# Kernel optimization log

Hardware: AMD Instinct MI355X
Metric: run time of the kernel (lower is better)

## Reference

```python
import jax, jax.numpy as jnp
import numpy as np

D = 256
RANK = 64
H = 8
DH = D // H
TOPK = 32  # top-k survivors per query row
NEG = -1e9


def lowrank(x, u, v):
    # x:[...,d] @ u:[d,rank] @ v:[rank,d]
    return (x @ u) @ v


def setup_inputs() -> dict:
    key = jax.random.key(0)
    ks = jax.random.split(key, 13)
    s_u = 1.0 / np.sqrt(D)
    s_v = 1.0 / np.sqrt(RANK)

    def pu(k):
        return jax.random.normal(k, (D, RANK), jnp.float32) * s_u

    def pv(k):
        return jax.random.normal(k, (RANK, D), jnp.float32) * s_v

    return {
        "x": jax.random.normal(ks[0], (2, 2048, D), jnp.float32),
        "ne_u": pu(ks[1]), "ne_v": pv(ks[2]),
        "wq_u": pu(ks[3]), "wq_v": pv(ks[4]),
        "wk_u": pu(ks[5]), "wk_v": pv(ks[6]),
        "wv_u": pu(ks[7]), "wv_v": pv(ks[8]),
        "wo_u": pu(ks[9]), "wo_v": pv(ks[10]),
        "es_u": pu(ks[11]), "es_v": pv(ks[12]),
    }


def reference(x, ne_u, ne_v, wq_u, wq_v, wk_u, wk_v, wv_u, wv_v, wo_u, wo_v, es_u, es_v):
    B, N, _ = x.shape
    # node embedding (low-rank projection)
    h = lowrank(x, ne_u, ne_v)  # [B,N,d]

    # low-rank multi-head Q/K/V
    def heads(t):  # [B,N,d] -> [B,H,N,dh]
        return t.reshape(B, N, H, DH).transpose(0, 2, 1, 3)

    q = heads(lowrank(h, wq_u, wq_v))
    k = heads(lowrank(h, wk_u, wk_v))
    v = heads(lowrank(h, wv_u, wv_v))

    scores = jnp.einsum("bhnd,bhmd->bhnm", q, k) / jnp.sqrt(jnp.float32(DH))
    # top-k sparsification per query row
    kth = jax.lax.top_k(scores, TOPK)[0][..., -1:]  # [B,H,N,1]
    masked = jnp.where(scores >= kth, scores, NEG)
    attn = jax.nn.softmax(masked, axis=-1)  # [B,H,N,N]

    out = jnp.einsum("bhnm,bhmd->bhnd", attn, v)  # [B,H,N,dh]
    out = out.transpose(0, 2, 1, 3).reshape(B, N, D)
    h2 = lowrank(out, wo_u, wo_v)  # output projection

    # edge scores -> adjacency with sigmoid + zero diagonal epilogue
    el = lowrank(h2, es_u, es_v)  # [B,N,d]
    adjacency = jax.nn.sigmoid(jnp.einsum("bnd,bmd->bnm", el, el))
    adjacency = adjacency * (1.0 - jnp.eye(N, dtype=adjacency.dtype))
    return adjacency, attn
```

## Files before the change

kernel.cpp:

```cpp
#include <hip/hip_runtime.h>
#include <hip/hip_bf16.h>
#include <cstdint>
#include <cstddef>

#define ATTN_OFF (2u*2048u*2048u)
#define SLOTS 48
#define DELTA 1e-3f
#define MAXB 16
#define CCAP 96

typedef __attribute__((ext_vector_type(8))) short bf16x8;
typedef __attribute__((ext_vector_type(4))) float f32x4;

__device__ __forceinline__ unsigned short bf16_hi(float f) {
  __hip_bfloat16 h = __float2bfloat16(f);
  return *(unsigned short*)&h;
}
__device__ __forceinline__ float bf16_val(unsigned short u) {
  __hip_bfloat16 h = *(__hip_bfloat16*)&u;
  return __bfloat162float(h);
}

__global__ __launch_bounds__(256) void fused_qkv_kernel(
    const float* __restrict__ x, const float* __restrict__ ne_u,
    const float* __restrict__ ne_v, const float* __restrict__ wq_u,
    const float* __restrict__ wq_v, const float* __restrict__ wk_u,
    const float* __restrict__ wk_v, const float* __restrict__ wv_u,
    const float* __restrict__ wv_v, double* __restrict__ qd,
    double* __restrict__ kd, unsigned short* __restrict__ qh,
    unsigned short* __restrict__ ql, unsigned short* __restrict__ kh,
    unsigned short* __restrict__ kl, float* __restrict__ v) {
  __shared__ double xm[4][64];
  __shared__ double hrow[4][256];
  __shared__ double mid2[4][64];

  int tid = threadIdx.x;
  int rr = tid >> 6;
  int j  = tid & 63;
  int row = blockIdx.x * 4 + rr;
  int b = row >> 11, m = row & 2047;
  const double INV = 0.17677669529663688110021109052621;

  const float* xr = x + (size_t)row * 256;
  {
    double a0 = 0, a1 = 0, a2 = 0, a3 = 0;
#pragma unroll 8
    for (int k4 = 0; k4 < 64; ++k4) {
      int kk = k4 * 4;
      a0 = fma((double)xr[kk + 0], (double)ne_u[(kk + 0) * 64 + j], a0);
      a1 = fma((double)xr[kk + 1], (double)ne_u[(kk + 1) * 64 + j], a1);
      a2 = fma((double)xr[kk + 2], (double)ne_u[(kk + 2) * 64 + j], a2);
      a3 = fma((double)xr[kk + 3], (double)ne_u[(kk + 3) * 64 + j], a3);
    }
    xm[rr][j] = (a0 + a1) + (a2 + a3);
  }
  __syncthreads();

#pragma unroll
  for (int cc = 0; cc < 4; ++cc) {
    int col = j + 64 * cc;
    double o0 = 0, o1 = 0, o2 = 0, o3 = 0;
#pragma unroll 4
    for (int r4 = 0; r4 < 16; ++r4) {
      int r = r4 * 4;
      o0 = fma(xm[rr][r + 0], (double)ne_v[(r + 0) * 256 + col], o0);
      o1 = fma(xm[rr][r + 1], (double)ne_v[(r + 1) * 256 + col], o1);
      o2 = fma(xm[rr][r + 2], (double)ne_v[(r + 2) * 256 + col], o2);
      o3 = fma(xm[rr][r + 3], (double)ne_v[(r + 3) * 256 + col], o3);
    }
    hrow[rr][col] = (o0 + o1) + (o2 + o3);
  }
  __syncthreads();

  for (int p = 0; p < 3; ++p) {
    const float* pu = (p == 0) ? wq_u : (p == 1) ? wk_u : wv_u;
    const float* pw = (p == 0) ? wq_v : (p == 1) ? wk_v : wv_v;

    double a0 = 0, a1 = 0, a2 = 0, a3 = 0;
#pragma unroll 8
    for (int k4 = 0; k4 < 64; ++k4) {
      int kk = k4 * 4;
      a0 = fma(hrow[rr][kk + 0], (double)pu[(kk + 0) * 64 + j], a0);
      a1 = fma(hrow[rr][kk + 1], (double)pu[(kk + 1) * 64 + j], a1);
      a2 = fma(hrow[rr][kk + 2], (double)pu[(kk + 2) * 64 + j], a2);
      a3 = fma(hrow[rr][kk + 3], (double)pu[(kk + 3) * 64 + j], a3);
    }
    mid2[rr][j] = (a0 + a1) + (a2 + a3);
    __syncthreads();

#pragma unroll
    for (int cc = 0; cc < 4; ++cc) {
      int col = j + 64 * cc;
      double o0 = 0, o1 = 0, o2 = 0, o3 = 0;
#pragma unroll 4
      for (int r4 = 0; r4 < 16; ++r4) {
        int r = r4 * 4;
        o0 = fma(mid2[rr][r + 0], (double)pw[(r + 0) * 256 + col], o0);
        o1 = fma(mid2[rr][r + 1], (double)pw[(r + 1) * 256 + col], o1);
        o2 = fma(mid2[rr][r + 2], (double)pw[(r + 2) * 256 + col], o2);
        o3 = fma(mid2[rr][r + 3], (double)pw[(r + 3) * 256 + col], o3);
      }
      double o = (o0 + o1) + (o2 + o3);
      if (p == 2) {
        v[(size_t)row * 256 + col] = (float)o;
      } else {
        int hh = col >> 5, d = col & 31;
        size_t haddr = (((size_t)(b * 8 + hh)) * 2048 + m) * 32 + d;
        if (p == 0) {
          qd[(size_t)row * 256 + col] = o;
          float f = (float)(o * INV);
          unsigned short hi = bf16_hi(f);
          float lof = f - bf16_val(hi);
          qh[haddr] = hi;
          ql[haddr] = bf16_hi(lof);
        } else {
          kd[(size_t)row * 256 + col] = o;
          float f = (float)o;
          unsigned short hi = bf16_hi(f);
          float lof = f - bf16_val(hi);
          kh[haddr] = hi;
          kl[haddr] = bf16_hi(lof);
        }
      }
    }
    __syncthreads();
  }
}

__global__ __launch_bounds__(512, 4) void attn_kernel(
    const unsigned short* __restrict__ qh, const unsigned short* __restrict__ ql,
    const unsigned short* __restrict__ kh, const unsigned short* __restrict__ kl,
    const double* __restrict__ qd, const double* __restrict__ kd,
    float* __restrict__ attn, float* __restrict__ pval,
    unsigned short* __restrict__ pidx) {
  __shared__ unsigned hist[16][64];
  __shared__ float cand[16][CCAP];
  __shared__ float sval[16][SLOTS];
  __shared__ unsigned short scol[16][SLOTS];
  __shared__ float rowmax_s[16][8];
  __shared__ unsigned c1_s[16][8];
  __shared__ unsigned c2_s[16][8];
  __shared__ float mx_s[16];
  __shared__ float kth_s[16];
  __shared__ float zinv_s[16];
  __shared__ float scale_s[16];
  __shared__ float thr_s[16];
  __shared__ int   kB_s[16];
  __shared__ unsigned kneed_s[16];
  __shared__ unsigned ccnt[16];
  __shared__ unsigned scnt[16];
  __shared__ unsigned chi_s[16];
  __shared__ unsigned bcnt[16];
  __shared__ unsigned short bidx[16][MAXB];
  __shared__ float bval[16][MAXB];
  __shared__ unsigned short bkeep[16][MAXB];
  __shared__ double bs64[16][MAXB];

  int tid = threadIdx.x;
  int bx  = blockIdx.x;
  int slab = bx >> 7;
  int rowtile = bx & 127;
  int b = slab >> 3, hh = slab & 7;
  int w = tid >> 6;
  int l = tid & 63;
  int g = l >> 4;
  int li = l & 15;
  const double INV64 = 0.17677669529663688110021109052621;

  size_t qoff = (((size_t)slab * 2048 + rowtile * 16 + li) * 32) + g * 8;
  bf16x8 a_hi = *(const bf16x8*)(qh + qoff);
  bf16x8 a_lo = *(const bf16x8*)(ql + qoff);

  float s[16][4];
  size_t kbase = ((size_t)slab * 2048 + w * 256 + li) * 32 + g * 8;
#pragma unroll
  for (int tt = 0; tt < 16; ++tt) {
    bf16x8 b_hi = *(const bf16x8*)(kh + kbase + (size_t)tt * 512);
    bf16x8 b_lo = *(const bf16x8*)(kl + kbase + (size_t)tt * 512);
    f32x4 acc = {0.f, 0.f, 0.f, 0.f};
    acc = __builtin_amdgcn_mfma_f32_16x16x32_bf16(a_hi, b_hi, acc, 0, 0, 0);
    acc = __builtin_amdgcn_mfma_f32_16x16x32_bf16(a_hi, b_lo, acc, 0, 0, 0);
    acc = __builtin_amdgcn_mfma_f32_16x16x32_bf16(a_lo, b_hi, acc, 0, 0, 0);
#pragma unroll
    for (int reg = 0; reg < 4; ++reg) s[tt][reg] = acc[reg];
  }

  for (int i = tid; i < 16 * 64; i += 512) ((unsigned*)hist)[i] = 0u;
  if (tid < 16) {
    ccnt[tid] = 0u; scnt[tid] = 0u; chi_s[tid] = 0u; bcnt[tid] = 0u;
    kth_s[tid] = -1e30f; kB_s[tid] = -1;
  }
  size_t prow0 = ((size_t)slab * 2048 + rowtile * 16);
  {
    float lmx[4];
#pragma unroll
    for (int reg = 0; reg < 4; ++reg) {
      float m = s[0][reg];
#pragma unroll
      for (int tt = 1; tt < 16; ++tt) m = fmaxf(m, s[tt][reg]);
      lmx[reg] = m;
    }
#pragma unroll
    for (int off = 1; off < 16; off <<= 1) {
#pragma unroll
      for (int reg = 0; reg < 4; ++reg)
        lmx[reg] = fmaxf(lmx[reg], __shfl_xor(lmx[reg], (unsigned)off, 16));
    }
    if (li == 0) {
#pragma unroll
      for (int reg = 0; reg < 4; ++reg) rowmax_s[4 * g + reg][w] = lmx[reg];
    }
  }
  __syncthreads();

  if (tid < 16) {
    float m = rowmax_s[tid][0];
#pragma unroll
    for (int i = 1; i < 8; ++i) m = fmaxf(m, rowmax_s[tid][i]);
    mx_s[tid] = m;
  }
  __syncthreads();

  {
    unsigned cc1[4], cc2[4];
#pragma unroll
    for (int reg = 0; reg < 4; ++reg) {
      float mx = mx_s[4 * g + reg];
      float t1 = mx - 1.0f, t2 = mx - 2.0f;
      unsigned a = 0, c = 0;
#pragma unroll
      for (int tt = 0; tt < 16; ++tt) {
        float v = s[tt][reg];
        a += (v >= t1) ? 1u : 0u;
        c += (v >= t2) ? 1u : 0u;
      }
      cc1[reg] = a; cc2[reg] = c;
    }
#pragma unroll
    for (int off = 1; off < 16; off <<= 1) {
#pragma unroll
      for (int reg = 0; reg < 4; ++reg) {
        cc1[reg] += (unsigned)__shfl_xor((int)cc1[reg], off, 16);
        cc2[reg] += (unsigned)__shfl_xor((int)cc2[reg], off, 16);
      }
    }
    if (li == 0) {
#pragma unroll
      for (int reg = 0; reg < 4; ++reg) {
        c1_s[4 * g + reg][w] = cc1[reg];
        c2_s[4 * g + reg][w] = cc2[reg];
      }
    }
  }
  __syncthreads();

  if (tid < 16) {
    unsigned t1 = 0, t2 = 0;
#pragma unroll
    for (int i = 0; i < 8; ++i) { t1 += c1_s[tid][i]; t2 += c2_s[tid][i]; }
    float scale, thr;
    if (t1 >= 32u)      { scale = 64.0f; thr = mx_s[tid] - 1.0f; }
    else if (t2 >= 32u) { scale = 32.0f; thr = mx_s[tid] - 2.0f; }
    else                { scale = 4.0f;  thr = -1e30f; }
    scale_s[tid] = scale; thr_s[tid] = thr;
  }
  __syncthreads();

#pragma unroll
  for (int reg = 0; reg < 4; ++reg) {
    int rloc = 4 * g + reg;
    float mx = mx_s[rloc], thr = thr_s[rloc], sc = scale_s[rloc];
#pragma unroll
    for (int tt = 0; tt < 16; ++tt) {
      float v = s[tt][reg];
      if (v >= thr) {
        int bb = (int)((mx - v) * sc);
        bb = bb > 63 ? 63 : bb;
        atomicAdd(&hist[rloc][bb], 1u);
      }
    }
  }
  __syncthreads();

  if (w < 4) {
    int rloc = w * 4 + g;
    unsigned cnt4 = 0;
#pragma unroll
    for (int i = 0; i < 4; ++i) cnt4 += hist[rloc][li * 4 + i];
    unsigned pre = cnt4;
#pragma unroll
    for (int off = 1; off < 16; off <<= 1) {
      unsigned t = __shfl_up(pre, (unsigned)off, 16);
      if (li >= off) pre += t;
    }
    unsigned excl = pre - cnt4;
    bool flag = (excl < 32u) && (pre >= 32u);
    unsigned long long bal = __ballot(flag);
    unsigned seg = (unsigned)((bal >> (g * 16)) & 0xFFFFull);
    if (flag) {
      int src = __ffs(seg) - 1;
      if (li == src) {
        unsigned cum = excl;
        int B = 63; unsigned cb = 0;
#pragma unroll
        for (int i = 0; i < 4; ++i) {
          unsigned hv = hist[rloc][li * 4 + i];
          if (cum < 32u && cum + hv >= 32u) { B = li * 4 + i; cb = cum; }
          cum += hv;
        }
        kB_s[rloc] = B;
        kneed_s[rloc] = 32u - cb;
      }
    }
  }
  __syncthreads();

#pragma unroll
  for (int reg = 0; reg < 4; ++reg) {
    int rloc = 4 * g + reg;
    float mx = mx_s[rloc], thr = thr_s[rloc], sc = scale_s[rloc];
    int kB = kB_s[rloc];
#pragma unroll
    for (int tt = 0; tt < 16; ++tt) {
      float v = s[tt][reg];
      if (v >= thr) {
        int bb = (int)((mx - v) * sc);
        bb = bb > 63 ? 63 : bb;
        if (bb == kB) {
          unsigned slot = atomicAdd(&ccnt[rloc], 1u);
          if (slot < (unsigned)CCAP) cand[rloc][slot] = v;
        }
      }
    }
  }
  __syncthreads();

  if (w < 4) {
    int rloc = w * 4 + g;
    unsigned n0 = ccnt[rloc];
    n0 = n0 > (unsigned)CCAP ? (unsigned)CCAP : n0;
    unsigned need = kneed_s[rloc];
    if (need > n0) need = n0;
    for (unsigned ci = (unsigned)li; ci < n0; ci += 16u) {
      float x = cand[rloc][ci];
      unsigned r = 0;
      for (unsigned jj = 0; jj < n0; ++jj) {
        float y = cand[rloc][jj];
        r += (y > x || (y == x && jj < ci)) ? 1u : 0u;
      }
      if (r == need - 1u) kth_s[rloc] = x;
    }
  }
  __syncthreads();

#pragma unroll
  for (int reg = 0; reg < 4; ++reg) {
    int rloc = 4 * g + reg;
    float kth = kth_s[rloc];
    unsigned cnt = 0;
#pragma unroll
    for (int tt = 0; tt < 16; ++tt) {
      float v = s[tt][reg];
      if (v > kth + DELTA) {
        ++cnt;
        unsigned slot = atomicAdd(&scnt[rloc], 1u);
        if (slot < (unsigned)SLOTS) {
          sval[rloc][slot] = v;
          scol[rloc][slot] = (unsigned short)(w * 256 + tt * 16 + li);
        }
      } else if (!(v < kth - DELTA)) {
        unsigned slot = atomicAdd(&bcnt[rloc], 1u);
        if (slot < (unsigned)MAXB) {
          bidx[rloc][slot] = (unsigned short)(w * 256 + tt * 16 + li);
          bval[rloc][slot] = v;
        }
      }
    }
#pragma unroll
    for (int off = 1; off < 16; off <<= 1)
      cnt += (unsigned)__shfl_xor((int)cnt, off, 16);
    if (li == 0) atomicAdd(&chi_s[rloc], cnt);
  }
  __syncthreads();

  if (w < 4) {
    int rloc = w * 4 + g;
    unsigned bn = bcnt[rloc];
    bn = bn > (unsigned)MAXB ? (unsigned)MAXB : bn;
    const double* qrow =
        qd + ((size_t)(b * 2048 + rowtile * 16 + rloc)) * 256 + hh * 32;
    for (unsigned ci = (unsigned)li; ci < bn; ci += 16u) {
      int m = bidx[rloc][ci];
      const double* krow = kd + ((size_t)(b * 2048 + m)) * 256 + hh * 32;
      double acc = 0.0;
#pragma unroll 8
      for (int d = 0; d < 32; ++d) acc = fma(qrow[d], krow[d], acc);
      bs64[rloc][ci] = acc * INV64;
    }
    unsigned need2 = 32u - chi_s[rloc];
    for (unsigned ci = (unsigned)li; ci < bn; ci += 16u) {
      double x = bs64[rloc][ci];
      unsigned r = 0;
      for (unsigned jj = 0; jj < bn; ++jj)
        r += (bs64[rloc][jj] > x) ? 1u : 0u;
      if (r < need2) {
        unsigned slot = atomicAdd(&scnt[rloc], 1u);
        if (slot < (unsigned)SLOTS) {
          sval[rloc][slot] = bval[rloc][ci];
          scol[rloc][slot] = bidx[rloc][ci];
        }
      }
    }
  }
  __syncthreads();

  float* base = attn + prow0 * 2048;
  if (w < 4) {
    int rloc = w * 4 + g;
    unsigned n = scnt[rloc];
    n = n > (unsigned)SLOTS ? (unsigned)SLOTS : n;
    float mx = mx_s[rloc];
    float z = 0.0f;
    for (unsigned i = (unsigned)li; i < n; i += 16u)
      z += __expf(sval[rloc][i] - mx);
#pragma unroll
    for (int off = 1; off < 16; off <<= 1) z += __shfl_xor(z, (unsigned)off, 16);
    if (li == 0) zinv_s[rloc] = 1.0f / z;
  } else {
    int t2 = tid - 256;
    f32x4 z4 = {0.f, 0.f, 0.f, 0.f};
#pragma unroll
    for (int it = 0; it < 32; ++it)
      __builtin_nontemporal_store(z4, ((f32x4*)base) + t2 + 256 * it);
  }
  __syncthreads();

  for (int e = tid; e < 16 * SLOTS; e += 512) {
    int rr = e / SLOTS, ii = e % SLOTS;
    unsigned n = scnt[rr];
    n = n > (unsigned)SLOTS ? (unsigned)SLOTS : n;
    float p = 0.0f;
    unsigned short c = 0;
    if ((unsigned)ii < n) {
      c = scol[rr][ii];
      p = __expf(sval[rr][ii] - mx_s[rr]) * zinv_s[rr];
      base[(size_t)rr * 2048 + c] = p;
    }
    pval[prow0 * SLOTS + e] = p;
    pidx[prow0 * SLOTS + e] = c;
  }
}

__global__ __launch_bounds__(256) void pv_wo_es_kernel(
    const float* __restrict__ pval, const unsigned short* __restrict__ pidx,
    const float* __restrict__ v,
    const float* __restrict__ wo_u, const float* __restrict__ wo_v,
    const float* __restrict__ es_u, const float* __restrict__ es_v,
    unsigned short* __restrict__ elh, unsigned short* __restrict__ ell) {
  __shared__ float svals[8][8][SLOTS];
  __shared__ unsigned short sidx[8][8][SLOTS];
  __shared__ float outr[8][256];
  __shared__ float mid[8][64];
  __shared__ float h2r[8][256];

  int tid = threadIdx.x;
  int bb = blockIdx.x >> 8;
  int rg = blockIdx.x & 255;
  int n0 = rg * 8;

  for (int e = tid; e < 8 * 8 * SLOTS; e += 256) {
    int rr = e / (8 * SLOTS);
    int rem = e % (8 * SLOTS);
    int hh = rem / SLOTS, ii = rem % SLOTS;
    size_t srow = ((size_t)(bb * 8 + hh) * 2048 + n0 + rr) * SLOTS + ii;
    svals[rr][hh][ii] = pval[srow];
    sidx[rr][hh][ii] = pidx[srow];
  }
  __syncthreads();

  {
    int d = tid, hh = d >> 5;
    const float* vb = v + (size_t)bb * 2048 * 256 + d;
    for (int r = 0; r < 8; ++r) {
      float acc = 0.f;
#pragma unroll 4
      for (int i = 0; i < SLOTS; ++i) {
        float p = svals[r][hh][i];
        int m = sidx[r][hh][i];
        acc = fmaf(p, vb[(size_t)m * 256], acc);
      }
      outr[r][d] = acc;
    }
  }
  __syncthreads();

  {
    int j = tid & 63, rb = tid >> 6;
    for (int r = rb; r < 8; r += 4) {
      float a0 = 0, a1 = 0, a2 = 0, a3 = 0;
#pragma unroll 8
      for (int k4 = 0; k4 < 64; ++k4) {
        int k = k4 * 4;
        a0 = fmaf(outr[r][k + 0], wo_u[(k + 0) * 64 + j], a0);
        a1 = fmaf(outr[r][k + 1], wo_u[(k + 1) * 64 + j], a1);
        a2 = fmaf(outr[r][k + 2], wo_u[(k + 2) * 64 + j], a2);
        a3 = fmaf(outr[r][k + 3], wo_u[(k + 3) * 64 + j], a3);
      }
      mid[r][j] = (a0 + a1) + (a2 + a3);
    }
  }
  __syncthreads();

  {
    int c = tid;
    for (int r = 0; r < 8; ++r) {
      float a0 = 0, a1 = 0, a2 = 0, a3 = 0;
#pragma unroll 4
      for (int k4 = 0; k4 < 16; ++k4) {
        int k = k4 * 4;
        a0 = fmaf(mid[r][k + 0], wo_v[(k + 0) * 256 + c], a0);
        a1 = fmaf(mid[r][k + 1], wo_v[(k + 1) * 256 + c], a1);
        a2 = fmaf(mid[r][k + 2], wo_v[(k + 2) * 256 + c], a2);
        a3 = fmaf(mid[r][k + 3], wo_v[(k + 3) * 256 + c], a3);
      }
      h2r[r][c] = (a0 + a1) + (a2 + a3);
    }
  }
  __syncthreads();

  {
    int j = tid & 63, rb = tid >> 6;
    for (int r = rb; r < 8; r += 4) {
      float a0 = 0, a1 = 0, a2 = 0, a3 = 0;
#pragma unroll 8
      for (int k4 = 0; k4 < 64; ++k4) {
        int k = k4 * 4;
        a0 = fmaf(h2r[r][k + 0], es_u[(k + 0) * 64 + j], a0);
        a1 = fmaf(h2r[r][k + 1], es_u[(k + 1) * 64 + j], a1);
        a2 = fmaf(h2r[r][k + 2], es_u[(k + 2) * 64 + j], a2);
        a3 = fmaf(h2r[r][k + 3], es_u[(k + 3) * 64 + j], a3);
      }
      mid[r][j] = (a0 + a1) + (a2 + a3);
    }
  }
  __syncthreads();

  {
    int c = tid;
    for (int r = 0; r < 8; ++r) {
      float a0 = 0, a1 = 0, a2 = 0, a3 = 0;
#pragma unroll 4
      for (int k4 = 0; k4 < 16; ++k4) {
        int k = k4 * 4;
        a0 = fmaf(mid[r][k + 0], es_v[(k + 0) * 256 + c], a0);
        a1 = fmaf(mid[r][k + 1], es_v[(k + 1) * 256 + c], a1);
        a2 = fmaf(mid[r][k + 2], es_v[(k + 2) * 256 + c], a2);
        a3 = fmaf(mid[r][k + 3], es_v[(k + 3) * 256 + c], a3);
      }
      float o = (a0 + a1) + (a2 + a3);
      size_t addr = ((size_t)(bb * 2048 + n0 + r)) * 256 + c;
      unsigned short hi = bf16_hi(o);
      elh[addr] = hi;
      ell[addr] = bf16_hi(o - bf16_val(hi));
    }
  }
}

__global__ __launch_bounds__(256) void adj_mfma_kernel(
    const unsigned short* __restrict__ elh, const unsigned short* __restrict__ ell,
    float* __restrict__ adj) {
  int tid = threadIdx.x;
  int l = tid & 63, w = tid >> 6;
  int li = l & 15, g = l >> 4;
  int b = blockIdx.z, rt = blockIdx.y, ct = blockIdx.x;

  int arow = rt * 64 + w * 16 + li;
  size_t abase = ((size_t)(b * 2048 + arow)) * 256 + g * 8;
  size_t bbase = ((size_t)(b * 2048 + ct * 64 + li)) * 256 + g * 8;

  f32x4 acc0 = {0.f, 0.f, 0.f, 0.f};
  f32x4 acc1 = {0.f, 0.f, 0.f, 0.f};
  f32x4 acc2 = {0.f, 0.f, 0.f, 0.f};
  f32x4 acc3 = {0.f, 0.f, 0.f, 0.f};

#pragma unroll
  for (int kc = 0; kc < 8; ++kc) {
    bf16x8 a_hi = *(const bf16x8*)(elh + abase + kc * 32);
    bf16x8 a_lo = *(const bf16x8*)(ell + abase + kc * 32);
#pragma unroll
    for (int t = 0; t < 4; ++t) {
      bf16x8 b_hi = *(const bf16x8*)(elh + bbase + (size_t)t * 16 * 256 + kc * 32);
      bf16x8 b_lo = *(const bf16x8*)(ell + bbase + (size_t)t * 16 * 256 + kc * 32);
      f32x4* pa = (t == 0) ? &acc0 : (t == 1) ? &acc1 : (t == 2) ? &acc2 : &acc3;
      *pa = __builtin_amdgcn_mfma_f32_16x16x32_bf16(a_hi, b_hi, *pa, 0, 0, 0);
      *pa = __builtin_amdgcn_mfma_f32_16x16x32_bf16(a_hi, b_lo, *pa, 0, 0, 0);
      *pa = __builtin_amdgcn_mfma_f32_16x16x32_bf16(a_lo, b_hi, *pa, 0, 0, 0);
    }
  }

  int orow0 = rt * 64 + w * 16 + g * 4;
#pragma unroll
  for (int t = 0; t < 4; ++t) {
    f32x4 a = (t == 0) ? acc0 : (t == 1) ? acc1 : (t == 2) ? acc2 : acc3;
    int cg = ct * 64 + t * 16 + li;
#pragma unroll
    for (int i = 0; i < 4; ++i) {
      int rg = orow0 + i;
      float sg = 1.0f / (1.0f + __expf(-a[i]));
      if (rg == cg) sg = 0.0f;
      adj[((size_t)b * 2048 + rg) * 2048 + cg] = sg;
    }
  }
}

extern "C" void kernel_launch(void* const* d_in, const int* in_sizes, int n_in,
                              void* d_out, int out_size, void* d_ws,
                              size_t ws_size, hipStream_t stream) {
  const float* x    = (const float*)d_in[0];
  const float* ne_u = (const float*)d_in[1];
  const float* ne_v = (const float*)d_in[2];
  const float* wq_u = (const float*)d_in[3];
  const float* wq_v = (const float*)d_in[4];
  const float* wk_u = (const float*)d_in[5];
  const float* wk_v = (const float*)d_in[6];
  const float* wv_u = (const float*)d_in[7];
  const float* wv_v = (const float*)d_in[8];
  const float* wo_u = (const float*)d_in[9];
  const float* wo_v = (const float*)d_in[10];
  const float* es_u = (const float*)d_in[11];
  const float* es_v = (const float*)d_in[12];

  float* adj  = (float*)d_out;
  float* attn = adj + (size_t)ATTN_OFF;

  char* ws = (char*)d_ws;
  double* qd = (double*)(ws);
  double* kd = (double*)(ws + ((size_t)8  << 20));
  unsigned short* qh = (unsigned short*)(ws + ((size_t)16 << 20));
  unsigned short* ql = (unsigned short*)(ws + ((size_t)18 << 20));
  unsigned short* kh = (unsigned short*)(ws + ((size_t)20 << 20));
  unsigned short* kl = (unsigned short*)(ws + ((size_t)22 << 20));
  float* v    = (float*)(ws + ((size_t)24 << 20));
  float* pval = (float*)(ws + ((size_t)28 << 20));
  unsigned short* pidx = (unsigned short*)(ws + ((size_t)35 << 20));
  unsigned short* elh = (unsigned short*)(ws + ((size_t)8  << 20));
  unsigned short* ell = (unsigned short*)(ws + ((size_t)10 << 20));

  fused_qkv_kernel<<<1024, 256, 0, stream>>>(
      x, ne_u, ne_v, wq_u, wq_v, wk_u, wk_v, wv_u, wv_v,
      qd, kd, qh, ql, kh, kl, v);

  attn_kernel<<<2048, 512, 0, stream>>>(qh, ql, kh, kl, qd, kd, attn, pval, pidx);
  pv_wo_es_kernel<<<512, 256, 0, stream>>>(pval, pidx, v, wo_u, wo_v,
                                           es_u, es_v, elh, ell);

  adj_mfma_kernel<<<dim3(32, 32, 2), 256, 0, stream>>>(elh, ell, adj);
}
```

Before: 395.7 us.

## Spread per-row top-k selection across all waves and halve rows per PV block

In the attention kernel, the threshold-count reduction now uses shared-memory atomics, so one barrier and a serial tid<16 pass go away. The histogram scan, candidate ranking, fp64 rescoring and softmax now run on all 8 waves with 32 lanes per row instead of 4 waves with 16 lanes. Exp values are cached in shared memory and reused for the normalised write, and the zero-fill of the output is spread across all threads. The PV/output-projection kernel processes 4 rows per block instead of 8, doubling the grid for more parallelism, at the cost of reloading the weights more often.

```diff
diff --git a/kernel.cpp b/kernel.cpp
--- a/kernel.cpp
+++ b/kernel.cpp
@@ -7,7 +7,8 @@
 #define SLOTS 48
 #define DELTA 1e-3f
 #define MAXB 16
-#define CCAP 96
+#define CCAP 64
+#define PVR 4
 
 typedef __attribute__((ext_vector_type(8))) short bf16x8;
 typedef __attribute__((ext_vector_type(4))) float f32x4;
@@ -138,22 +139,18 @@
   __shared__ float sval[16][SLOTS];
   __shared__ unsigned short scol[16][SLOTS];
   __shared__ float rowmax_s[16][8];
-  __shared__ unsigned c1_s[16][8];
-  __shared__ unsigned c2_s[16][8];
   __shared__ float mx_s[16];
   __shared__ float kth_s[16];
   __shared__ float zinv_s[16];
-  __shared__ float scale_s[16];
-  __shared__ float thr_s[16];
   __shared__ int   kB_s[16];
   __shared__ unsigned kneed_s[16];
+  __shared__ unsigned c1t[16], c2t[16];
   __shared__ unsigned ccnt[16];
   __shared__ unsigned scnt[16];
   __shared__ unsigned chi_s[16];
   __shared__ unsigned bcnt[16];
   __shared__ unsigned short bidx[16][MAXB];
   __shared__ float bval[16][MAXB];
-  __shared__ unsigned short bkeep[16][MAXB];
   __shared__ double bs64[16][MAXB];
 
   int tid = threadIdx.x;
@@ -165,6 +162,9 @@
   int l = tid & 63;
   int g = l >> 4;
   int li = l & 15;
+  int h32 = l >> 5;
+  int c32 = l & 31;
+  int rw = w * 2 + h32;
   const double INV64 = 0.17677669529663688110021109052621;
 
   size_t qoff = (((size_t)slab * 2048 + rowtile * 16 + li) * 32) + g * 8;
@@ -188,6 +188,7 @@
   for (int i = tid; i < 16 * 64; i += 512) ((unsigned*)hist)[i] = 0u;
   if (tid < 16) {
     ccnt[tid] = 0u; scnt[tid] = 0u; chi_s[tid] = 0u; bcnt[tid] = 0u;
+    c1t[tid] = 0u; c2t[tid] = 0u;
     kth_s[tid] = -1e30f; kB_s[tid] = -1;
   }
   size_t prow0 = ((size_t)slab * 2048 + rowtile * 16);
@@ -222,10 +223,10 @@
   __syncthreads();
 
   {
-    unsigned cc1[4], cc2[4];
 #pragma unroll
     for (int reg = 0; reg < 4; ++reg) {
-      float mx = mx_s[4 * g + reg];
+      int rloc = 4 * g + reg;
+      float mx = mx_s[rloc];
       float t1 = mx - 1.0f, t2 = mx - 2.0f;
       unsigned a = 0, c = 0;
 #pragma unroll
@@ -234,42 +235,28 @@
         a += (v >= t1) ? 1u : 0u;
         c += (v >= t2) ? 1u : 0u;
       }
-      cc1[reg] = a; cc2[reg] = c;
-    }
-#pragma unroll
-    for (int off = 1; off < 16; off <<= 1) {
-#pragma unroll
-      for (int reg = 0; reg < 4; ++reg) {
-        cc1[reg] += (unsigned)__shfl_xor((int)cc1[reg], off, 16);
-        cc2[reg] += (unsigned)__shfl_xor((int)cc2[reg], off, 16);
-      }
-    }
-    if (li == 0) {
-#pragma unroll
-      for (int reg = 0; reg < 4; ++reg) {
-        c1_s[4 * g + reg][w] = cc1[reg];
-        c2_s[4 * g + reg][w] = cc2[reg];
-      }
-    }
-  }
-  __syncthreads();
-
-  if (tid < 16) {
-    unsigned t1 = 0, t2 = 0;
-#pragma unroll
-    for (int i = 0; i < 8; ++i) { t1 += c1_s[tid][i]; t2 += c2_s[tid][i]; }
-    float scale, thr;
-    if (t1 >= 32u)      { scale = 64.0f; thr = mx_s[tid] - 1.0f; }
-    else if (t2 >= 32u) { scale = 32.0f; thr = mx_s[tid] - 2.0f; }
-    else                { scale = 4.0f;  thr = -1e30f; }
-    scale_s[tid] = scale; thr_s[tid] = thr;
+#pragma unroll
+      for (int off = 1; off < 16; off <<= 1) {
+        a += (unsigned)__shfl_xor((int)a, off, 16);
+        c += (unsigned)__shfl_xor((int)c, off, 16);
+      }
+      if (li == 0) {
+        if (a) atomicAdd(&c1t[rloc], a);
+        if (c) atomicAdd(&c2t[rloc], c);
+      }
+    }
   }
   __syncthreads();
 
 #pragma unroll
   for (int reg = 0; reg < 4; ++reg) {
     int rloc = 4 * g + reg;
-    float mx = mx_s[rloc], thr = thr_s[rloc], sc = scale_s[rloc];
+    float mx = mx_s[rloc];
+    unsigned t1 = c1t[rloc], t2 = c2t[rloc];
+    float sc, thr;
+    if (t1 >= 32u)      { sc = 64.0f; thr = mx - 1.0f; }
+    else if (t2 >= 32u) { sc = 32.0f; thr = mx - 2.0f; }
+    else                { sc = 4.0f;  thr = -1e30f; }
 #pragma unroll
     for (int tt = 0; tt < 16; ++tt) {
       float v = s[tt][reg];
@@ -282,34 +269,31 @@
   }
   __syncthreads();
 
-  if (w < 4) {
-    int rloc = w * 4 + g;
-    unsigned cnt4 = 0;
-#pragma unroll
-    for (int i = 0; i < 4; ++i) cnt4 += hist[rloc][li * 4 + i];
-    unsigned pre = cnt4;
-#pragma unroll
-    for (int off = 1; off < 16; off <<= 1) {
-      unsigned t = __shfl_up(pre, (unsigned)off, 16);
-      if (li >= off) pre += t;
-    }
-    unsigned excl = pre - cnt4;
+  {
+    unsigned cnt2 = hist[rw][c32 * 2] + hist[rw][c32 * 2 + 1];
+    unsigned pre = cnt2;
+#pragma unroll
+    for (int off = 1; off < 32; off <<= 1) {
+      unsigned t = __shfl_up(pre, (unsigned)off, 32);
+      if (c32 >= off) pre += t;
+    }
+    unsigned excl = pre - cnt2;
     bool flag = (excl < 32u) && (pre >= 32u);
     unsigned long long bal = __ballot(flag);
-    unsigned seg = (unsigned)((bal >> (g * 16)) & 0xFFFFull);
+    unsigned seg = (unsigned)((bal >> (h32 * 32)) & 0xFFFFFFFFull);
     if (flag) {
       int src = __ffs(seg) - 1;
-      if (li == src) {
+      if (c32 == src) {
         unsigned cum = excl;
         int B = 63; unsigned cb = 0;
 #pragma unroll
-        for (int i = 0; i < 4; ++i) {
-          unsigned hv = hist[rloc][li * 4 + i];
-          if (cum < 32u && cum + hv >= 32u) { B = li * 4 + i; cb = cum; }
+        for (int i = 0; i < 2; ++i) {
+          unsigned hv = hist[rw][c32 * 2 + i];
+          if (cum < 32u && cum + hv >= 32u) { B = c32 * 2 + i; cb = cum; }
           cum += hv;
         }
-        kB_s[rloc] = B;
-        kneed_s[rloc] = 32u - cb;
+        kB_s[rw] = B;
+        kneed_s[rw] = 32u - cb;
       }
     }
   }
@@ -318,7 +302,12 @@
 #pragma unroll
   for (int reg = 0; reg < 4; ++reg) {
     int rloc = 4 * g + reg;
-    float mx = mx_s[rloc], thr = thr_s[rloc], sc = scale_s[rloc];
+    float mx = mx_s[rloc];
+    unsigned t1 = c1t[rloc], t2 = c2t[rloc];
+    float sc, thr;
+    if (t1 >= 32u)      { sc = 64.0f; thr = mx - 1.0f; }
+    else if (t2 >= 32u) { sc = 32.0f; thr = mx - 2.0f; }
+    else                { sc = 4.0f;  thr = -1e30f; }
     int kB = kB_s[rloc];
 #pragma unroll
     for (int tt = 0; tt < 16; ++tt) {
@@ -335,20 +324,19 @@
   }
   __syncthreads();
 
-  if (w < 4) {
-    int rloc = w * 4 + g;
-    unsigned n0 = ccnt[rloc];
+  {
+    unsigned n0 = ccnt[rw];
     n0 = n0 > (unsigned)CCAP ? (unsigned)CCAP : n0;
-    unsigned need = kneed_s[rloc];
+    unsigned need = kneed_s[rw];
     if (need > n0) need = n0;
-    for (unsigned ci = (unsigned)li; ci < n0; ci += 16u) {
-      float x = cand[rloc][ci];
+    for (unsigned ci = (unsigned)c32; ci < n0; ci += 32u) {
+      float x = cand[rw][ci];
       unsigned r = 0;
       for (unsigned jj = 0; jj < n0; ++jj) {
-        float y = cand[rloc][jj];
+        float y = cand[rw][jj];
         r += (y > x || (y == x && jj < ci)) ? 1u : 0u;
       }
-      if (r == need - 1u) kth_s[rloc] = x;
+      if (r == need - 1u) kth_s[rw] = x;
     }
   }
   __syncthreads();
@@ -379,35 +367,34 @@
 #pragma unroll
     for (int off = 1; off < 16; off <<= 1)
       cnt += (unsigned)__shfl_xor((int)cnt, off, 16);
-    if (li == 0) atomicAdd(&chi_s[rloc], cnt);
-  }
-  __syncthreads();
-
-  if (w < 4) {
-    int rloc = w * 4 + g;
-    unsigned bn = bcnt[rloc];
+    if (li == 0 && cnt) atomicAdd(&chi_s[rloc], cnt);
+  }
+  __syncthreads();
+
+  {
+    unsigned bn = bcnt[rw];
     bn = bn > (unsigned)MAXB ? (unsigned)MAXB : bn;
     const double* qrow =
-        qd + ((size_t)(b * 2048 + rowtile * 16 + rloc)) * 256 + hh * 32;
-    for (unsigned ci = (unsigned)li; ci < bn; ci += 16u) {
-      int m = bidx[rloc][ci];
+        qd + ((size_t)(b * 2048 + rowtile * 16 + rw)) * 256 + hh * 32;
+    for (unsigned ci = (unsigned)c32; ci < bn; ci += 32u) {
+      int m = bidx[rw][ci];
       const double* krow = kd + ((size_t)(b * 2048 + m)) * 256 + hh * 32;
       double acc = 0.0;
 #pragma unroll 8
       for (int d = 0; d < 32; ++d) acc = fma(qrow[d], krow[d], acc);
-      bs64[rloc][ci] = acc * INV64;
-    }
-    unsigned need2 = 32u - chi_s[rloc];
-    for (unsigned ci = (unsigned)li; ci < bn; ci += 16u) {
-      double x = bs64[rloc][ci];
+      bs64[rw][ci] = acc * INV64;
+    }
+    unsigned need2 = 32u - chi_s[rw];
+    for (unsigned ci = (unsigned)c32; ci < bn; ci += 32u) {
+      double x = bs64[rw][ci];
       unsigned r = 0;
       for (unsigned jj = 0; jj < bn; ++jj)
-        r += (bs64[rloc][jj] > x) ? 1u : 0u;
+        r += (bs64[rw][jj] > x) ? 1u : 0u;
       if (r < need2) {
-        unsigned slot = atomicAdd(&scnt[rloc], 1u);
+        unsigned slot = atomicAdd(&scnt[rw], 1u);
         if (slot < (unsigned)SLOTS) {
-          sval[rloc][slot] = bval[rloc][ci];
-          scol[rloc][slot] = bidx[rloc][ci];
+          sval[rw][slot] = bval[rw][ci];
+          scol[rw][slot] = bidx[rw][ci];
         }
       }
     }
@@ -415,23 +402,25 @@
   __syncthreads();
 
   float* base = attn + prow0 * 2048;
-  if (w < 4) {
-    int rloc = w * 4 + g;
-    unsigned n = scnt[rloc];
+  {
+    unsigned n = scnt[rw];
     n = n > (unsigned)SLOTS ? (unsigned)SLOTS : n;
-    float mx = mx_s[rloc];
+    float mx = mx_s[rw];
     float z = 0.0f;
-    for (unsigned i = (unsigned)li; i < n; i += 16u)
-      z += __expf(sval[rloc][i] - mx);
-#pragma unroll
-    for (int off = 1; off < 16; off <<= 1) z += __shfl_xor(z, (unsigned)off, 16);
-    if (li == 0) zinv_s[rloc] = 1.0f / z;
-  } else {
-    int t2 = tid - 256;
+    for (unsigned i = (unsigned)c32; i < n; i += 32u) {
+      float e = __expf(sval[rw][i] - mx);
+      sval[rw][i] = e;
+      z += e;
+    }
+#pragma unroll
+    for (int off = 1; off < 32; off <<= 1) z += __shfl_xor(z, (unsigned)off, 32);
+    if (c32 == 0) zinv_s[rw] = 1.0f / z;
+  }
+  {
     f32x4 z4 = {0.f, 0.f, 0.f, 0.f};
 #pragma unroll
-    for (int it = 0; it < 32; ++it)
-      __builtin_nontemporal_store(z4, ((f32x4*)base) + t2 + 256 * it);
+    for (int it = 0; it < 16; ++it)
+      __builtin_nontemporal_store(z4, ((f32x4*)base) + tid + 512 * it);
   }
   __syncthreads();
 
@@ -443,7 +432,7 @@
     unsigned short c = 0;
     if ((unsigned)ii < n) {
       c = scol[rr][ii];
-      p = __expf(sval[rr][ii] - mx_s[rr]) * zinv_s[rr];
+      p = sval[rr][ii] * zinv_s[rr];
       base[(size_t)rr * 2048 + c] = p;
     }
     pval[prow0 * SLOTS + e] = p;
@@ -457,18 +446,18 @@
     const float* __restrict__ wo_u, const float* __restrict__ wo_v,
     const float* __restrict__ es_u, const float* __restrict__ es_v,
     unsigned short* __restrict__ elh, unsigned short* __restrict__ ell) {
-  __shared__ float svals[8][8][SLOTS];
-  __shared__ unsigned short sidx[8][8][SLOTS];
-  __shared__ float outr[8][256];
-  __shared__ float mid[8][64];
-  __shared__ float h2r[8][256];
+  __shared__ float svals[PVR][8][SLOTS];
+  __shared__ unsigned short sidx[PVR][8][SLOTS];
+  __shared__ float outr[PVR][256];
+  __shared__ float mid[PVR][64];
+  __shared__ float h2r[PVR][256];
 
   int tid = threadIdx.x;
-  int bb = blockIdx.x >> 8;
-  int rg = blockIdx.x & 255;
-  int n0 = rg * 8;
-
-  for (int e = tid; e < 8 * 8 * SLOTS; e += 256) {
+  int bb = blockIdx.x >> 9;
+  int rg = blockIdx.x & 511;
+  int n0 = rg * PVR;
+
+  for (int e = tid; e < PVR * 8 * SLOTS; e += 256) {
     int rr = e / (8 * SLOTS);
     int rem = e % (8 * SLOTS);
     int hh = rem / SLOTS, ii = rem % SLOTS;
@@ -481,7 +470,7 @@
   {
     int d = tid, hh = d >> 5;
     const float* vb = v + (size_t)bb * 2048 * 256 + d;
-    for (int r = 0; r < 8; ++r) {
+    for (int r = 0; r < PVR; ++r) {
       float acc = 0.f;
 #pragma unroll 4
       for (int i = 0; i < SLOTS; ++i) {
@@ -496,7 +485,7 @@
 
   {
     int j = tid & 63, rb = tid >> 6;
-    for (int r = rb; r < 8; r += 4) {
+    for (int r = rb; r < PVR; r += 4) {
       float a0 = 0, a1 = 0, a2 = 0, a3 = 0;
 #pragma unroll 8
       for (int k4 = 0; k4 < 64; ++k4) {
@@ -513,7 +502,7 @@
 
   {
     int c = tid;
-    for (int r = 0; r < 8; ++r) {
+    for (int r = 0; r < PVR; ++r) {
       float a0 = 0, a1 = 0, a2 = 0, a3 = 0;
 #pragma unroll 4
       for (int k4 = 0; k4 < 16; ++k4) {
@@ -530,7 +519,7 @@
 
   {
     int j = tid & 63, rb = tid >> 6;
-    for (int r = rb; r < 8; r += 4) {
+    for (int r = rb; r < PVR; r += 4) {
       float a0 = 0, a1 = 0, a2 = 0, a3 = 0;
 #pragma unroll 8
       for (int k4 = 0; k4 < 64; ++k4) {
@@ -547,7 +536,7 @@
 
   {
     int c = tid;
-    for (int r = 0; r < 8; ++r) {
+    for (int r = 0; r < PVR; ++r) {
       float a0 = 0, a1 = 0, a2 = 0, a3 = 0;
 #pragma unroll 4
       for (int k4 = 0; k4 < 16; ++k4) {
@@ -651,8 +640,8 @@
       qd, kd, qh, ql, kh, kl, v);
 
   attn_kernel<<<2048, 512, 0, stream>>>(qh, ql, kh, kl, qd, kd, attn, pval, pidx);
-  pv_wo_es_kernel<<<512, 256, 0, stream>>>(pval, pidx, v, wo_u, wo_v,
-                                           es_u, es_v, elh, ell);
+  pv_wo_es_kernel<<<1024, 256, 0, stream>>>(pval, pidx, v, wo_u, wo_v,
+                                            es_u, es_v, elh, ell);
 
   adj_mfma_kernel<<<dim3(32, 32, 2), 256, 0, stream>>>(elh, ell, adj);
 }
```

Measured after the change: 387.5 us. 2.1% less time.
